# Performance work log

Measured on AMD Instinct MI355X. Metric: run time of the kernel, lower is better.

## Reference

```python
import jax, jax.numpy as jnp
import numpy as np

B, T, D, H1, H2, O = 64, 256, 512, 1024, 1024, 512


def setup_inputs() -> dict:
    key = jax.random.key(0)
    ks = jax.random.split(key, 6)
    s = 0.05  # weight scale for numerical sanity
    return {
        "x": jax.random.normal(ks[0], (B, T, D), dtype=jnp.float32),
        "W1": jax.random.normal(ks[1], (D, 4 * H1), dtype=jnp.float32) * s,
        "U1": jax.random.normal(ks[2], (H1, 4 * H1), dtype=jnp.float32) * s,
        "b1": jnp.zeros((4 * H1,), dtype=jnp.float32),
        "W2": jax.random.normal(ks[3], (H1, 4 * H2), dtype=jnp.float32) * s,
        "U2": jax.random.normal(ks[4], (H2, 4 * H2), dtype=jnp.float32) * s,
        "b2": jnp.zeros((4 * H2,), dtype=jnp.float32),
        "Wd": jax.random.normal(ks[5], (H2, O), dtype=jnp.float32) * s,
        "bd": jnp.zeros((O,), dtype=jnp.float32),
    }


def _lstm_layer(x_seq, W, U, b, units):
    """Run an LSTM layer over x_seq [B,T,Din]; returns full h sequence [B,T,units].

    Keras LSTMCell gate order: i, f, c(g), o; sigmoid recurrent activation, tanh activation.
    """
    # Precompute input projections for all timesteps: [T, B, 4*units]
    xz = (jnp.einsum('btd,dk->tbk', x_seq, W) + b).astype(x_seq.dtype)
    bsz = x_seq.shape[0]
    h0 = jnp.zeros((bsz, units), dtype=x_seq.dtype)
    c0 = jnp.zeros((bsz, units), dtype=x_seq.dtype)

    def step(carry, xz_t):
        h, c = carry
        z = xz_t + h @ U
        zi, zf, zg, zo = jnp.split(z, 4, axis=-1)
        c_new = jax.nn.sigmoid(zf) * c + jax.nn.sigmoid(zi) * jnp.tanh(zg)
        h_new = jax.nn.sigmoid(zo) * jnp.tanh(c_new)
        return (h_new, c_new), h_new

    (_, _), hs = jax.lax.scan(step, (h0, c0), xz)  # hs: [T, B, units]
    return jnp.transpose(hs, (1, 0, 2))


def reference(x, W1, U1, b1, W2, U2, b2, Wd, bd):
    seq1 = _lstm_layer(x, W1, U1, b1, H1)          # [B, T, H1]
    seq2 = _lstm_layer(seq1, W2, U2, b2, H2)       # [B, T, H2]
    h_last = seq2[:, -1, :]                        # final hidden state of layer 2
    return h_last @ Wd + bd
```

## Files before the change

kernel.cpp:

```cpp
#include <hip/hip_runtime.h>


typedef __bf16 bf16x8 __attribute__((ext_vector_type(8)));
typedef float f32x4 __attribute__((ext_vector_type(4)));
typedef unsigned int u32x4 __attribute__((ext_vector_type(4)));
typedef unsigned short u16;

#define LDS_Z_OFF 131584
#define LDS_TOTAL 140288

__device__ __forceinline__ u16 f2bf(float f) {
  unsigned u = __float_as_uint(f);
  unsigned r = (u + 0x7FFFu + ((u >> 16) & 1u)) >> 16;
  return (u16)r;
}

__global__ __launch_bounds__(256) void transpose_to_bf16(
    const float* __restrict__ in, u16* __restrict__ out, int R, int C) {
  __shared__ float tile[32][33];
  int tx = threadIdx.x & 31, ty = threadIdx.x >> 5;
  int c0 = blockIdx.x * 32, r0 = blockIdx.y * 32;
#pragma unroll
  for (int i = 0; i < 4; ++i)
    tile[ty + i * 8][tx] = in[(size_t)(r0 + ty + i * 8) * C + (c0 + tx)];
  __syncthreads();
#pragma unroll
  for (int i = 0; i < 4; ++i)
    out[(size_t)(c0 + ty + i * 8) * R + (r0 + tx)] = f2bf(tile[tx][ty + i * 8]);
}

__global__ __launch_bounds__(256) void convert_to_bf16(
    const float* __restrict__ in, u16* __restrict__ out, int n4) {
  int i = blockIdx.x * 256 + threadIdx.x;
  if (i >= n4) return;
  float4 v = reinterpret_cast<const float4*>(in)[i];
  ushort4 o;
  o.x = f2bf(v.x); o.y = f2bf(v.y); o.z = f2bf(v.z); o.w = f2bf(v.w);
  reinterpret_cast<ushort4*>(out)[i] = o;
}

__global__ void init_bar(unsigned* __restrict__ bar) { bar[threadIdx.x] = 0u; }

__device__ __forceinline__ void store_h_sc1(u16* p, unsigned v) {
  asm volatile("global_store_short %0, %1, off sc1" :: "v"(p), "v"(v) : "memory");
}

template <int I, int C0, int DEPTH, bool SC0, bool SC1>
__device__ __forceinline__ void stg_issue(u32x4 (&ring)[DEPTH],
    const u16* b0, const u16* b1) {
  constexpr int OFF = (I < C0 ? I : I - C0) * 128;
  if constexpr (I < C0) {
    if constexpr (SC0)
      asm volatile("global_load_dwordx4 %0, %1, off offset:%2 sc1"
                   : "=v"(ring[I % DEPTH]) : "v"(b0), "i"(OFF));
    else
      asm volatile("global_load_dwordx4 %0, %1, off offset:%2"
                   : "=v"(ring[I % DEPTH]) : "v"(b0), "i"(OFF));
  } else {
    if constexpr (SC1)
      asm volatile("global_load_dwordx4 %0, %1, off offset:%2 sc1"
                   : "=v"(ring[I % DEPTH]) : "v"(b1), "i"(OFF));
    else
      asm volatile("global_load_dwordx4 %0, %1, off offset:%2"
                   : "=v"(ring[I % DEPTH]) : "v"(b1), "i"(OFF));
  }
}

template <int I, int NPRE, int C0, int DEPTH, bool SC0, bool SC1>
__device__ __forceinline__ void stg_pre(u32x4 (&ring)[DEPTH],
    const u16* b0, const u16* b1) {
  if constexpr (I < NPRE) {
    stg_issue<I, C0, DEPTH, SC0, SC1>(ring, b0, b1);
    stg_pre<I + 1, NPRE, C0, DEPTH, SC0, SC1>(ring, b0, b1);
  }
}

template <int I, int NC, int C0, int DEPTH, bool SC0, bool SC1>
__device__ __forceinline__ void stg_main(u32x4 (&ring)[DEPTH],
    const u16* b0, const u16* b1, u16* lrow) {
  if constexpr (I < NC) {
    constexpr int ISSUED = (I + DEPTH < NC) ? I + DEPTH : NC;
    constexpr int WAIT = ISSUED - I - 1;
    asm volatile("s_waitcnt vmcnt(%1)" : "+v"(ring[I % DEPTH]) : "i"(WAIT));
    *(u32x4*)(lrow + I * 64) = ring[I % DEPTH];
    if constexpr (I + DEPTH < NC)
      stg_issue<I + DEPTH, C0, DEPTH, SC0, SC1>(ring, b0, b1);
    stg_main<I + 1, NC, C0, DEPTH, SC0, SC1>(ring, b0, b1, lrow);
  }
}

template <int NC, int C0, bool SC0, bool SC1>
__device__ __forceinline__ void stage(const u16* b0, const u16* b1, u16* lrow) {
  u32x4 ring[16];
  stg_pre<0, (NC < 16 ? NC : 16), C0, 16, SC0, SC1>(ring, b0, b1);
  stg_main<0, NC, C0, 16, SC0, SC1>(ring, b0, b1, lrow);
}

__device__ __forceinline__ void grid_barrier(unsigned* __restrict__ bar,
                                             int g, unsigned want) {
  asm volatile("s_waitcnt vmcnt(0)" ::: "memory");
  __syncthreads();
  if (threadIdx.x == 0) {
    unsigned old = __hip_atomic_fetch_add(bar + 32 * (1 + g), 1u,
                                          __ATOMIC_RELAXED, __HIP_MEMORY_SCOPE_AGENT);
    if (old == 32u * want - 1u) {
      unsigned r = __hip_atomic_fetch_add(bar, 1u, __ATOMIC_RELAXED,
                                          __HIP_MEMORY_SCOPE_AGENT);
      if (r == 8u * want - 1u) {
#pragma unroll
        for (int i = 0; i < 8; ++i)
          __hip_atomic_store(bar + 32 * (9 + i), want, __ATOMIC_RELAXED,
                             __HIP_MEMORY_SCOPE_AGENT);
      }
    }
    while (__hip_atomic_load(bar + 32 * (9 + g), __ATOMIC_RELAXED,
                             __HIP_MEMORY_SCOPE_AGENT) < want)
      __builtin_amdgcn_s_sleep(1);
  }
  __syncthreads();
}

template <int NC, int C0, bool SC0, bool IS2>
__device__ __forceinline__ void run_layer(
    const u16* __restrict__ xbf, const u16* __restrict__ Wt,
    const u16* __restrict__ Ut, const float* __restrict__ bias,
    u16* __restrict__ h1r, u16* __restrict__ h2r, unsigned* __restrict__ bar,
    int strip, int mhalf, char* smem, int g) {
  constexpr int K = NC * 64;
  constexpr int P = K + 8;
  constexpr int NCH = NC * 2;
  constexpr int WCH = C0 * 2;
  u16* Alds = (u16*)smem;
  float* Zlds = (float*)(smem + LDS_Z_OFF);
  const int tid = threadIdx.x;
  const int wave = tid >> 6, lane = tid & 63;
  const int quad = lane >> 4, l16 = lane & 15;

  bf16x8 breg[NCH];
  const int col = wave * 1024 + strip * 16 + l16;
#pragma unroll
  for (int ks = 0; ks < WCH; ++ks)
    breg[ks] = *(const bf16x8*)(Wt + (size_t)col * (C0 * 64) + ks * 32 + quad * 8);
#pragma unroll
  for (int ks = WCH; ks < NCH; ++ks)
    breg[ks] = *(const bf16x8*)(Ut + (size_t)col * 1024 + (ks - WCH) * 32 + quad * 8);

  const int eu = tid & 15, em = tid >> 4;
  const float bz0 = bias[strip * 16 + eu];
  const float bz1 = bias[1024 + strip * 16 + eu];
  const float bz2 = bias[2048 + strip * 16 + eu];
  const float bz3 = bias[3072 + strip * 16 + eu];
  float cA = 0.f, cB = 0.f;

  const int sr = tid >> 3, l8 = tid & 7;
  const int sb = mhalf * 32 + sr;
  u16* lrow = Alds + sr * P + l8 * 8;

  const u16* a0p = Alds + l16 * P + quad * 8;
  const u16* a1p = a0p + 16 * P;

  for (int s = 0; s <= 256; ++s) {
    const int t = IS2 ? (s - 1) : s;
    if (t >= 0 && t < 256) {
      const u16 *b0, *b1;
      if constexpr (IS2) {
        b0 = h1r + (size_t)(t & 1) * 65536 + (size_t)sb * 1024 + l8 * 8;
        b1 = h2r + (size_t)((t - 1) & 1) * 65536 + (size_t)sb * 1024 + l8 * 8;
      } else {
        b0 = xbf + ((size_t)sb * 256 + t) * 512 + l8 * 8;
        b1 = h1r + (size_t)((t - 1) & 1) * 65536 + (size_t)sb * 1024 + l8 * 8;
      }
      if (t > 0) {
        stage<NC, C0, SC0, true>(b0, b1, lrow);
      } else {
        stage<C0, C0, SC0, true>(b0, b0, lrow);
#pragma unroll
        for (int i = C0; i < NC; ++i)
          *(u32x4*)(lrow + i * 64) = (u32x4){0u, 0u, 0u, 0u};
      }
      __syncthreads();

      f32x4 acc0 = {0.f, 0.f, 0.f, 0.f}, acc1 = {0.f, 0.f, 0.f, 0.f};
#pragma unroll
      for (int ks = 0; ks < NCH; ++ks) {
        bf16x8 a0 = *(const bf16x8*)(a0p + ks * 32);
        bf16x8 a1 = *(const bf16x8*)(a1p + ks * 32);
        acc0 = __builtin_amdgcn_mfma_f32_16x16x32_bf16(a0, breg[ks], acc0, 0, 0, 0);
        acc1 = __builtin_amdgcn_mfma_f32_16x16x32_bf16(a1, breg[ks], acc1, 0, 0, 0);
      }

#pragma unroll
      for (int i = 0; i < 4; ++i) {
        Zlds[(quad * 4 + i) * 68 + wave * 16 + l16] = acc0[i];
        Zlds[(16 + quad * 4 + i) * 68 + wave * 16 + l16] = acc1[i];
      }
      __syncthreads();

      u16* hring = IS2 ? h2r : h1r;
      u16* hp = hring + (size_t)(t & 1) * 65536 +
                (size_t)(mhalf * 32) * 1024 + strip * 16 + eu;
      {
        float zi = Zlds[em * 68 + eu] + bz0;
        float zf = Zlds[em * 68 + 16 + eu] + bz1;
        float zg = Zlds[em * 68 + 32 + eu] + bz2;
        float zo = Zlds[em * 68 + 48 + eu] + bz3;
        float ig = 1.f / (1.f + __expf(-zi));
        float fg = 1.f / (1.f + __expf(-zf));
        float gg = 1.f - 2.f / (1.f + __expf(2.f * zg));
        float og = 1.f / (1.f + __expf(-zo));
        cA = fg * cA + ig * gg;
        float h = og * (1.f - 2.f / (1.f + __expf(2.f * cA)));
        store_h_sc1(hp + (size_t)em * 1024, (unsigned)f2bf(h));
      }
      {
        int m2 = em + 16;
        float zi = Zlds[m2 * 68 + eu] + bz0;
        float zf = Zlds[m2 * 68 + 16 + eu] + bz1;
        float zg = Zlds[m2 * 68 + 32 + eu] + bz2;
        float zo = Zlds[m2 * 68 + 48 + eu] + bz3;
        float ig = 1.f / (1.f + __expf(-zi));
        float fg = 1.f / (1.f + __expf(-zf));
        float gg = 1.f - 2.f / (1.f + __expf(2.f * zg));
        float og = 1.f / (1.f + __expf(-zo));
        cB = fg * cB + ig * gg;
        float h = og * (1.f - 2.f / (1.f + __expf(2.f * cB)));
        store_h_sc1(hp + (size_t)m2 * 1024, (unsigned)f2bf(h));
      }
    }
    if (s < 256) grid_barrier(bar, g, (unsigned)(s + 1));
  }
}

__global__ __launch_bounds__(256, 1) void lstm_persistent(
    const u16* __restrict__ xbf,
    const u16* __restrict__ W1t,
    const u16* __restrict__ U1t,
    const float* __restrict__ b1,
    const u16* __restrict__ W2t,
    const u16* __restrict__ U2t,
    const float* __restrict__ b2,
    u16* __restrict__ h1r,
    u16* __restrict__ h2r,
    unsigned* __restrict__ bar) {
  extern __shared__ __align__(16) char smem[];
  const int blk = blockIdx.x;
  const bool is2 = blk >= 128;
  const int lb = is2 ? blk - 128 : blk;
  const int strip = lb >> 1;
  const int mhalf = lb & 1;
  const int g = blk & 7;
  if (!is2)
    run_layer<24, 8, false, false>(xbf, W1t, U1t, b1, h1r, h2r, bar,
                                   strip, mhalf, smem, g);
  else
    run_layer<32, 16, true, true>(xbf, W2t, U2t, b2, h1r, h2r, bar,
                                  strip, mhalf, smem, g);
}

__global__ __launch_bounds__(64) void dense_kernel(
    const u16* __restrict__ h2,
    const u16* __restrict__ Wdt,
    const float* __restrict__ bd,
    float* __restrict__ out) {
  int mt = blockIdx.x >> 5;
  int nt = blockIdx.x & 31;
  int lane = threadIdx.x;
  int quad = lane >> 4, l16 = lane & 15;
  f32x4 acc = {0.f, 0.f, 0.f, 0.f};
  const u16* ap = h2 + (size_t)(mt * 16 + l16) * 1024 + quad * 8;
  const u16* bp = Wdt + (size_t)(nt * 16 + l16) * 1024 + quad * 8;
#pragma unroll
  for (int ks = 0; ks < 32; ++ks) {
    bf16x8 a = *reinterpret_cast<const bf16x8*>(ap + ks * 32);
    bf16x8 b = *reinterpret_cast<const bf16x8*>(bp + ks * 32);
    acc = __builtin_amdgcn_mfma_f32_16x16x32_bf16(a, b, acc, 0, 0, 0);
  }
  int colo = nt * 16 + l16;
  float bias = bd[colo];
#pragma unroll
  for (int i = 0; i < 4; ++i)
    out[(size_t)(mt * 16 + quad * 4 + i) * 512 + colo] = acc[i] + bias;
}

extern "C" void kernel_launch(void* const* d_in, const int* in_sizes, int n_in,
                              void* d_out, int out_size, void* d_ws, size_t ws_size,
                              hipStream_t stream) {
  const float* x  = (const float*)d_in[0];
  const float* W1 = (const float*)d_in[1];
  const float* U1 = (const float*)d_in[2];
  const float* b1 = (const float*)d_in[3];
  const float* W2 = (const float*)d_in[4];
  const float* U2 = (const float*)d_in[5];
  const float* b2 = (const float*)d_in[6];
  const float* Wd = (const float*)d_in[7];
  const float* bd = (const float*)d_in[8];
  float* out = (float*)d_out;

  char* p = (char*)d_ws;
  auto carve = [&](size_t bytes) -> char* {
    char* r = p;
    p += (bytes + 255) & ~(size_t)255;
    return r;
  };
  u16* W1t = (u16*)carve((size_t)4096 * 512 * 2);
  u16* U1t = (u16*)carve((size_t)4096 * 1024 * 2);
  u16* W2t = (u16*)carve((size_t)4096 * 1024 * 2);
  u16* U2t = (u16*)carve((size_t)4096 * 1024 * 2);
  u16* Wdt = (u16*)carve((size_t)512 * 1024 * 2);
  u16* xbf = (u16*)carve((size_t)64 * 256 * 512 * 2);
  u16* h1r = (u16*)carve((size_t)2 * 64 * 1024 * 2);
  u16* h2r = (u16*)carve((size_t)2 * 64 * 1024 * 2);
  unsigned* bar = (unsigned*)carve(1024 * 4);
  (void)ws_size; (void)in_sizes; (void)n_in; (void)out_size;

  transpose_to_bf16<<<dim3(128, 16), 256, 0, stream>>>(W1, W1t, 512, 4096);
  transpose_to_bf16<<<dim3(128, 32), 256, 0, stream>>>(U1, U1t, 1024, 4096);
  transpose_to_bf16<<<dim3(128, 32), 256, 0, stream>>>(W2, W2t, 1024, 4096);
  transpose_to_bf16<<<dim3(128, 32), 256, 0, stream>>>(U2, U2t, 1024, 4096);
  transpose_to_bf16<<<dim3(16, 32), 256, 0, stream>>>(Wd, Wdt, 1024, 512);
  convert_to_bf16<<<8192, 256, 0, stream>>>(x, xbf, 64 * 256 * 512 / 4);
  init_bar<<<1, 1024, 0, stream>>>(bar);

  hipFuncSetAttribute(reinterpret_cast<const void*>(lstm_persistent),
                      hipFuncAttributeMaxDynamicSharedMemorySize, LDS_TOTAL);
  lstm_persistent<<<256, 256, LDS_TOTAL, stream>>>(
      xbf, W1t, U1t, b1, W2t, U2t, b2, h1r, h2r, bar);

  dense_kernel<<<128, 64, 0, stream>>>(h2r + 65536, Wdt, bd, out);
}
```

Measured before the change: 1.655 ms.

## Overlap staged activation loads with MFMA compute in four K-chunks per step

The per-step staging of the input and hidden-state rows into LDS is split into four spans. After each span a block barrier runs, and the MFMAs for that quarter of K are issued while the later loads are still in flight. This targets the serial load-then-compute latency on the recurrent critical path. It adds three extra __syncthreads per step and assumes NC is at least 16 and divisible by 4.

```diff
diff --git a/kernel.cpp b/kernel.cpp
--- a/kernel.cpp
+++ b/kernel.cpp
@@ -75,17 +75,17 @@
   }
 }
 
-template <int I, int NC, int C0, int DEPTH, bool SC0, bool SC1>
-__device__ __forceinline__ void stg_main(u32x4 (&ring)[DEPTH],
+template <int I, int END, int NC, int C0, int DEPTH, bool SC0, bool SC1>
+__device__ __forceinline__ void stg_span(u32x4 (&ring)[DEPTH],
     const u16* b0, const u16* b1, u16* lrow) {
-  if constexpr (I < NC) {
+  if constexpr (I < END) {
     constexpr int ISSUED = (I + DEPTH < NC) ? I + DEPTH : NC;
     constexpr int WAIT = ISSUED - I - 1;
     asm volatile("s_waitcnt vmcnt(%1)" : "+v"(ring[I % DEPTH]) : "i"(WAIT));
     *(u32x4*)(lrow + I * 64) = ring[I % DEPTH];
     if constexpr (I + DEPTH < NC)
       stg_issue<I + DEPTH, C0, DEPTH, SC0, SC1>(ring, b0, b1);
-    stg_main<I + 1, NC, C0, DEPTH, SC0, SC1>(ring, b0, b1, lrow);
+    stg_span<I + 1, END, NC, C0, DEPTH, SC0, SC1>(ring, b0, b1, lrow);
   }
 }
 
@@ -93,7 +93,7 @@
 __device__ __forceinline__ void stage(const u16* b0, const u16* b1, u16* lrow) {
   u32x4 ring[16];
   stg_pre<0, (NC < 16 ? NC : 16), C0, 16, SC0, SC1>(ring, b0, b1);
-  stg_main<0, NC, C0, 16, SC0, SC1>(ring, b0, b1, lrow);
+  stg_span<0, NC, NC, C0, 16, SC0, SC1>(ring, b0, b1, lrow);
 }
 
 __device__ __forceinline__ void grid_barrier(unsigned* __restrict__ bar,
@@ -130,6 +130,8 @@
   constexpr int P = K + 8;
   constexpr int NCH = NC * 2;
   constexpr int WCH = C0 * 2;
+  constexpr int NPS = NC / 4;
+  constexpr int NCHS = NCH / 4;
   u16* Alds = (u16*)smem;
   float* Zlds = (float*)(smem + LDS_Z_OFF);
   const int tid = threadIdx.x;
@@ -158,6 +160,17 @@
 
   const u16* a0p = Alds + l16 * P + quad * 8;
   const u16* a1p = a0p + 16 * P;
+
+#define MFMA_RNG(LO, HI)                                                     \
+  {                                                                          \
+    _Pragma("unroll")                                                        \
+    for (int ks = (LO); ks < (HI); ++ks) {                                   \
+      bf16x8 a0 = *(const bf16x8*)(a0p + ks * 32);                           \
+      bf16x8 a1 = *(const bf16x8*)(a1p + ks * 32);                           \
+      acc0 = __builtin_amdgcn_mfma_f32_16x16x32_bf16(a0, breg[ks], acc0, 0, 0, 0); \
+      acc1 = __builtin_amdgcn_mfma_f32_16x16x32_bf16(a1, breg[ks], acc1, 0, 0, 0); \
+    }                                                                        \
+  }
 
   for (int s = 0; s <= 256; ++s) {
     const int t = IS2 ? (s - 1) : s;
@@ -170,23 +183,30 @@
         b0 = xbf + ((size_t)sb * 256 + t) * 512 + l8 * 8;
         b1 = h1r + (size_t)((t - 1) & 1) * 65536 + (size_t)sb * 1024 + l8 * 8;
       }
+
+      f32x4 acc0 = {0.f, 0.f, 0.f, 0.f}, acc1 = {0.f, 0.f, 0.f, 0.f};
       if (t > 0) {
-        stage<NC, C0, SC0, true>(b0, b1, lrow);
+        u32x4 ring[16];
+        stg_pre<0, 16, C0, 16, SC0, true>(ring, b0, b1);
+        stg_span<0, NPS, NC, C0, 16, SC0, true>(ring, b0, b1, lrow);
+        __syncthreads();
+        MFMA_RNG(0, NCHS);
+        stg_span<NPS, 2 * NPS, NC, C0, 16, SC0, true>(ring, b0, b1, lrow);
+        __syncthreads();
+        MFMA_RNG(NCHS, 2 * NCHS);
+        stg_span<2 * NPS, 3 * NPS, NC, C0, 16, SC0, true>(ring, b0, b1, lrow);
+        __syncthreads();
+        MFMA_RNG(2 * NCHS, 3 * NCHS);
+        stg_span<3 * NPS, NC, NC, C0, 16, SC0, true>(ring, b0, b1, lrow);
+        __syncthreads();
+        MFMA_RNG(3 * NCHS, NCH);
       } else {
         stage<C0, C0, SC0, true>(b0, b0, lrow);
 #pragma unroll
         for (int i = C0; i < NC; ++i)
           *(u32x4*)(lrow + i * 64) = (u32x4){0u, 0u, 0u, 0u};
-      }
-      __syncthreads();
-
-      f32x4 acc0 = {0.f, 0.f, 0.f, 0.f}, acc1 = {0.f, 0.f, 0.f, 0.f};
-#pragma unroll
-      for (int ks = 0; ks < NCH; ++ks) {
-        bf16x8 a0 = *(const bf16x8*)(a0p + ks * 32);
-        bf16x8 a1 = *(const bf16x8*)(a1p + ks * 32);
-        acc0 = __builtin_amdgcn_mfma_f32_16x16x32_bf16(a0, breg[ks], acc0, 0, 0, 0);
-        acc1 = __builtin_amdgcn_mfma_f32_16x16x32_bf16(a1, breg[ks], acc1, 0, 0, 0);
+        __syncthreads();
+        MFMA_RNG(0, NCH);
       }
 
 #pragma unroll
@@ -229,6 +249,7 @@
     }
     if (s < 256) grid_barrier(bar, g, (unsigned)(s + 1));
   }
+#undef MFMA_RNG
 }
 
 __global__ __launch_bounds__(256, 1) void lstm_persistent(
```

Result: slower. 2.114 ms (+27.7%).

## Split LSTM step K dimension across two wave groups with 512-thread blocks

Applied to the files above, without the earlier changes.

Doubles the block size to 512 threads so that eight waves each compute one gate over half of the K range, and the two partial sums are reduced through LDS before the gate math. The staging loads now use 16 threads per row with a shallower prefetch ring, and each thread handles one output row instead of two. The goal is to halve per-wave MFMA chain length and register-held weights, which shortens the serial critical path of each timestep. In exchange it adds an LDS reduction and more LDS, and the launch_bounds(512,2) hint may not be achievable given the shared memory footprint.

```diff
diff --git a/kernel.cpp b/kernel.cpp
--- a/kernel.cpp
+++ b/kernel.cpp
@@ -7,7 +7,7 @@
 typedef unsigned short u16;
 
 #define LDS_Z_OFF 131584
-#define LDS_TOTAL 140288
+#define LDS_TOTAL 148992
 
 __device__ __forceinline__ u16 f2bf(float f) {
   unsigned u = __float_as_uint(f);
@@ -48,7 +48,7 @@
 template <int I, int C0, int DEPTH, bool SC0, bool SC1>
 __device__ __forceinline__ void stg_issue(u32x4 (&ring)[DEPTH],
     const u16* b0, const u16* b1) {
-  constexpr int OFF = (I < C0 ? I : I - C0) * 128;
+  constexpr int OFF = (I < C0 ? I : I - C0) * 256;
   if constexpr (I < C0) {
     if constexpr (SC0)
       asm volatile("global_load_dwordx4 %0, %1, off offset:%2 sc1"
@@ -82,7 +82,7 @@
     constexpr int ISSUED = (I + DEPTH < NC) ? I + DEPTH : NC;
     constexpr int WAIT = ISSUED - I - 1;
     asm volatile("s_waitcnt vmcnt(%1)" : "+v"(ring[I % DEPTH]) : "i"(WAIT));
-    *(u32x4*)(lrow + I * 64) = ring[I % DEPTH];
+    *(u32x4*)(lrow + I * 128) = ring[I % DEPTH];
     if constexpr (I + DEPTH < NC)
       stg_issue<I + DEPTH, C0, DEPTH, SC0, SC1>(ring, b0, b1);
     stg_main<I + 1, NC, C0, DEPTH, SC0, SC1>(ring, b0, b1, lrow);
@@ -91,9 +91,9 @@
 
 template <int NC, int C0, bool SC0, bool SC1>
 __device__ __forceinline__ void stage(const u16* b0, const u16* b1, u16* lrow) {
-  u32x4 ring[16];
-  stg_pre<0, (NC < 16 ? NC : 16), C0, 16, SC0, SC1>(ring, b0, b1);
-  stg_main<0, NC, C0, 16, SC0, SC1>(ring, b0, b1, lrow);
+  u32x4 ring[8];
+  stg_pre<0, (NC < 8 ? NC : 8), C0, 8, SC0, SC1>(ring, b0, b1);
+  stg_main<0, NC, C0, 8, SC0, SC1>(ring, b0, b1, lrow);
 }
 
 __device__ __forceinline__ void grid_barrier(unsigned* __restrict__ bar,
@@ -126,37 +126,42 @@
     const u16* __restrict__ Ut, const float* __restrict__ bias,
     u16* __restrict__ h1r, u16* __restrict__ h2r, unsigned* __restrict__ bar,
     int strip, int mhalf, char* smem, int g) {
-  constexpr int K = NC * 64;
-  constexpr int P = K + 8;
-  constexpr int NCH = NC * 2;
-  constexpr int WCH = C0 * 2;
+  constexpr int KE = NC * 128;
+  constexpr int P = KE + 8;
+  constexpr int NCH = NC * 4;
+  constexpr int WCH = C0 * 4;
+  constexpr int HALF = NCH / 2;
   u16* Alds = (u16*)smem;
   float* Zlds = (float*)(smem + LDS_Z_OFF);
   const int tid = threadIdx.x;
   const int wave = tid >> 6, lane = tid & 63;
+  const int gate = wave & 3, kh = wave >> 2;
   const int quad = lane >> 4, l16 = lane & 15;
 
-  bf16x8 breg[NCH];
-  const int col = wave * 1024 + strip * 16 + l16;
-#pragma unroll
-  for (int ks = 0; ks < WCH; ++ks)
-    breg[ks] = *(const bf16x8*)(Wt + (size_t)col * (C0 * 64) + ks * 32 + quad * 8);
-#pragma unroll
-  for (int ks = WCH; ks < NCH; ++ks)
-    breg[ks] = *(const bf16x8*)(Ut + (size_t)col * 1024 + (ks - WCH) * 32 + quad * 8);
+  bf16x8 breg[HALF];
+  const int col = gate * 1024 + strip * 16 + l16;
+  const int kb = kh * HALF;
+#pragma unroll
+  for (int j = 0; j < HALF; ++j) {
+    int ks = kb + j;
+    if (ks < WCH)
+      breg[j] = *(const bf16x8*)(Wt + (size_t)col * (WCH * 32) + ks * 32 + quad * 8);
+    else
+      breg[j] = *(const bf16x8*)(Ut + (size_t)col * 1024 + (ks - WCH) * 32 + quad * 8);
+  }
 
   const int eu = tid & 15, em = tid >> 4;
   const float bz0 = bias[strip * 16 + eu];
   const float bz1 = bias[1024 + strip * 16 + eu];
   const float bz2 = bias[2048 + strip * 16 + eu];
   const float bz3 = bias[3072 + strip * 16 + eu];
-  float cA = 0.f, cB = 0.f;
-
-  const int sr = tid >> 3, l8 = tid & 7;
+  float c = 0.f;
+
+  const int sr = tid >> 4, l8 = tid & 15;
   const int sb = mhalf * 32 + sr;
   u16* lrow = Alds + sr * P + l8 * 8;
 
-  const u16* a0p = Alds + l16 * P + quad * 8;
+  const u16* a0p = Alds + l16 * P + quad * 8 + kb * 32;
   const u16* a1p = a0p + 16 * P;
 
   for (int s = 0; s <= 256; ++s) {
@@ -176,62 +181,49 @@
         stage<C0, C0, SC0, true>(b0, b0, lrow);
 #pragma unroll
         for (int i = C0; i < NC; ++i)
-          *(u32x4*)(lrow + i * 64) = (u32x4){0u, 0u, 0u, 0u};
+          *(u32x4*)(lrow + i * 128) = (u32x4){0u, 0u, 0u, 0u};
       }
       __syncthreads();
 
       f32x4 acc0 = {0.f, 0.f, 0.f, 0.f}, acc1 = {0.f, 0.f, 0.f, 0.f};
 #pragma unroll
-      for (int ks = 0; ks < NCH; ++ks) {
-        bf16x8 a0 = *(const bf16x8*)(a0p + ks * 32);
-        bf16x8 a1 = *(const bf16x8*)(a1p + ks * 32);
-        acc0 = __builtin_amdgcn_mfma_f32_16x16x32_bf16(a0, breg[ks], acc0, 0, 0, 0);
-        acc1 = __builtin_amdgcn_mfma_f32_16x16x32_bf16(a1, breg[ks], acc1, 0, 0, 0);
-      }
-
+      for (int j = 0; j < HALF; ++j) {
+        bf16x8 a0 = *(const bf16x8*)(a0p + j * 32);
+        bf16x8 a1 = *(const bf16x8*)(a1p + j * 32);
+        acc0 = __builtin_amdgcn_mfma_f32_16x16x32_bf16(a0, breg[j], acc0, 0, 0, 0);
+        acc1 = __builtin_amdgcn_mfma_f32_16x16x32_bf16(a1, breg[j], acc1, 0, 0, 0);
+      }
+
+      float* zb = Zlds + kh * (32 * 68);
 #pragma unroll
       for (int i = 0; i < 4; ++i) {
-        Zlds[(quad * 4 + i) * 68 + wave * 16 + l16] = acc0[i];
-        Zlds[(16 + quad * 4 + i) * 68 + wave * 16 + l16] = acc1[i];
+        zb[(quad * 4 + i) * 68 + gate * 16 + l16] = acc0[i];
+        zb[(16 + quad * 4 + i) * 68 + gate * 16 + l16] = acc1[i];
       }
       __syncthreads();
 
       u16* hring = IS2 ? h2r : h1r;
       u16* hp = hring + (size_t)(t & 1) * 65536 +
-                (size_t)(mhalf * 32) * 1024 + strip * 16 + eu;
+                (size_t)(mhalf * 32 + em) * 1024 + strip * 16 + eu;
       {
-        float zi = Zlds[em * 68 + eu] + bz0;
-        float zf = Zlds[em * 68 + 16 + eu] + bz1;
-        float zg = Zlds[em * 68 + 32 + eu] + bz2;
-        float zo = Zlds[em * 68 + 48 + eu] + bz3;
+        float zi = Zlds[em * 68 + eu]      + Zlds[(32 + em) * 68 + eu]      + bz0;
+        float zf = Zlds[em * 68 + 16 + eu] + Zlds[(32 + em) * 68 + 16 + eu] + bz1;
+        float zg = Zlds[em * 68 + 32 + eu] + Zlds[(32 + em) * 68 + 32 + eu] + bz2;
+        float zo = Zlds[em * 68 + 48 + eu] + Zlds[(32 + em) * 68 + 48 + eu] + bz3;
         float ig = 1.f / (1.f + __expf(-zi));
         float fg = 1.f / (1.f + __expf(-zf));
         float gg = 1.f - 2.f / (1.f + __expf(2.f * zg));
         float og = 1.f / (1.f + __expf(-zo));
-        cA = fg * cA + ig * gg;
-        float h = og * (1.f - 2.f / (1.f + __expf(2.f * cA)));
-        store_h_sc1(hp + (size_t)em * 1024, (unsigned)f2bf(h));
-      }
-      {
-        int m2 = em + 16;
-        float zi = Zlds[m2 * 68 + eu] + bz0;
-        float zf = Zlds[m2 * 68 + 16 + eu] + bz1;
-        float zg = Zlds[m2 * 68 + 32 + eu] + bz2;
-        float zo = Zlds[m2 * 68 + 48 + eu] + bz3;
-        float ig = 1.f / (1.f + __expf(-zi));
-        float fg = 1.f / (1.f + __expf(-zf));
-        float gg = 1.f - 2.f / (1.f + __expf(2.f * zg));
-        float og = 1.f / (1.f + __expf(-zo));
-        cB = fg * cB + ig * gg;
-        float h = og * (1.f - 2.f / (1.f + __expf(2.f * cB)));
-        store_h_sc1(hp + (size_t)m2 * 1024, (unsigned)f2bf(h));
+        c = fg * c + ig * gg;
+        float h = og * (1.f - 2.f / (1.f + __expf(2.f * c)));
+        store_h_sc1(hp, (unsigned)f2bf(h));
       }
     }
     if (s < 256) grid_barrier(bar, g, (unsigned)(s + 1));
   }
 }
 
-__global__ __launch_bounds__(256, 1) void lstm_persistent(
+__global__ __launch_bounds__(512, 2) void lstm_persistent(
     const u16* __restrict__ xbf,
     const u16* __restrict__ W1t,
     const u16* __restrict__ U1t,
@@ -250,11 +242,11 @@
   const int mhalf = lb & 1;
   const int g = blk & 7;
   if (!is2)
-    run_layer<24, 8, false, false>(xbf, W1t, U1t, b1, h1r, h2r, bar,
+    run_layer<12, 4, false, false>(xbf, W1t, U1t, b1, h1r, h2r, bar,
                                    strip, mhalf, smem, g);
   else
-    run_layer<32, 16, true, true>(xbf, W2t, U2t, b2, h1r, h2r, bar,
-                                  strip, mhalf, smem, g);
+    run_layer<16, 8, true, true>(xbf, W2t, U2t, b2, h1r, h2r, bar,
+                                 strip, mhalf, smem, g);
 }
 
 __global__ __launch_bounds__(64) void dense_kernel(
@@ -323,7 +315,7 @@
 
   hipFuncSetAttribute(reinterpret_cast<const void*>(lstm_persistent),
                       hipFuncAttributeMaxDynamicSharedMemorySize, LDS_TOTAL);
-  lstm_persistent<<<256, 256, LDS_TOTAL, stream>>>(
+  lstm_persistent<<<256, 512, LDS_TOTAL, stream>>>(
       xbf, W1t, U1t, b1, W2t, U2t, b2, h1r, h2r, bar);
 
   dense_kernel<<<128, 64, 0, stream>>>(h2r + 65536, Wdt, bd, out);
```

Result: no change. 1.623 ms (-1.9%).
